# Kernel optimization log

Measured on AMD Instinct MI355X. Metric: run time of the kernel, lower is better.

The kernel has to match this reference:

```python
import jax, jax.numpy as jnp
import numpy as np

B, C, H, W = 4, 512, 64, 64
D = 512  # model_dim


def setup_inputs() -> dict:
    key = jax.random.key(0)
    ks = jax.random.split(key, 9)
    s = 0.02
    return {
        "q": jax.random.normal(ks[0], (B, C, H, W), dtype=jnp.float32),
        "Wq": jax.random.normal(ks[1], (D, C), dtype=jnp.float32) * s,
        "bq": jax.random.normal(ks[2], (D,), dtype=jnp.float32) * s,
        "Wk": jax.random.normal(ks[3], (D, C), dtype=jnp.float32) * s,
        "bk": jax.random.normal(ks[4], (D,), dtype=jnp.float32) * s,
        "Wv": jax.random.normal(ks[5], (D, C), dtype=jnp.float32) * s,
        "bv": jax.random.normal(ks[6], (D,), dtype=jnp.float32) * s,
        "Wo": jax.random.normal(ks[7], (C, D), dtype=jnp.float32) * s,
        "bo": jax.random.normal(ks[8], (C,), dtype=jnp.float32) * s,
    }


def reference(q, Wq, bq, Wk, bk, Wv, bv, Wo, bo):
    b, c, h, w = q.shape
    # 1x1 conv == per-pixel linear over channels; tokens s = h*w
    x = q.reshape(b, c, h * w)                      # (b, c, s)
    Q = jnp.einsum('bcs,dc->bsd', x, Wq) + bq       # (b, s, D)
    K = jnp.einsum('bcs,dc->bsd', x, Wk) + bk
    V = jnp.einsum('bcs,dc->bsd', x, Wv) + bv
    # ScaleAttend: scale = q.shape[-1]^-0.5 = model_dim^-0.5 (heads not split)
    scale = jnp.asarray(Q.shape[-1], Q.dtype) ** -0.5
    sim = jnp.einsum('bsd,btd->bst', Q, K) * scale  # (b, s, s)
    attn = jax.nn.softmax(sim, axis=-1)
    o = jnp.einsum('bst,btd->bsd', attn, V)         # (b, s, D)
    # to_out 1x1 conv: D -> C
    y = jnp.einsum('bsd,cd->bsc', o, Wo) + bo       # (b, s, C)
    return y.transpose(0, 2, 1).reshape(b, c, h, w)
```

## Files before the change

### kernel.cpp

```cpp
#include <hip/hip_runtime.h>
#include <hip/hip_bf16.h>

typedef __hip_bfloat16 bf16;
typedef __attribute__((ext_vector_type(8))) short short8;
typedef __attribute__((ext_vector_type(4))) float floatx4;
typedef __attribute__((ext_vector_type(4))) short shortx4;

static constexpr int BATCH = 4;
static constexpr int CH    = 512;
static constexpr int SEQ   = 4096;
static constexpr int DM    = 512;

__device__ __forceinline__ void gload16(const void* g, void* l) {
  __builtin_amdgcn_global_load_lds(
      (const __attribute__((address_space(1))) unsigned int*)g,
      (__attribute__((address_space(3))) unsigned int*)l,
      16, 0, 0);
}

__device__ __forceinline__ float hw_exp2(float x) {
  float r;
  asm("v_exp_f32 %0, %1" : "=v"(r) : "v"(x));
  return r;
}

__global__ __launch_bounds__(256) void cvt_weights(
    const float* __restrict__ w0, const float* __restrict__ w1,
    const float* __restrict__ w2, const float* __restrict__ w3,
    bf16* __restrict__ out) {
  const float* src = (blockIdx.y == 0) ? w0 : (blockIdx.y == 1) ? w1
                   : (blockIdx.y == 2) ? w2 : w3;
  int idx = blockIdx.x * 256 + threadIdx.x;
  out[(long)blockIdx.y * (DM * CH) + idx] = __float2bfloat16(src[idx]);
}

__global__ __launch_bounds__(256) void transpose_cvt(
    const float* __restrict__ x, bf16* __restrict__ xT) {
  __shared__ float tile[64][65];
  const int s0 = blockIdx.x * 64, c0 = blockIdx.y * 64;
  const float* xb = x + (long)blockIdx.z * CH * SEQ;
  bf16* xTb = xT + (long)blockIdx.z * SEQ * CH;
  const int t = threadIdx.x;
  const int sl = t & 63, cq = t >> 6;
  #pragma unroll
  for (int i = 0; i < 16; ++i) {
    int cl = cq * 16 + i;
    tile[cl][sl] = xb[(long)(c0 + cl) * SEQ + s0 + sl];
  }
  __syncthreads();
  const int cl2 = t & 63, sq = t >> 6;
  #pragma unroll
  for (int i = 0; i < 16; ++i) {
    int sl2 = sq * 16 + i;
    xTb[(long)(s0 + sl2) * CH + c0 + cl2] = __float2bfloat16(tile[cl2][sl2]);
  }
}

__global__ __launch_bounds__(512, 2) void gemm_qk(
    const bf16* __restrict__ A, long sAz,
    const bf16* __restrict__ B, long sBz,
    bf16* __restrict__ C, long sCz,
    float scale, int K, int ldc) {
  __shared__ __align__(16) bf16 As[2][256 * 64];
  __shared__ __align__(16) bf16 Bs[2][256 * 64];

  int id = blockIdx.x + gridDim.x * (blockIdx.y + gridDim.y * blockIdx.z);
  int nwg = gridDim.x * gridDim.y * gridDim.z;
  int sid = ((nwg & 7) == 0) ? ((id & 7) * (nwg >> 3) + (id >> 3)) : id;
  const int bx = sid % gridDim.x;
  const int by = (sid / gridDim.x) % gridDim.y;
  const int bz = sid / (gridDim.x * gridDim.y);

  const int tid = threadIdx.x;
  const long lK = K;
  const bf16* Ab = A + (long)bz * sAz + (long)by * 256 * lK;
  const bf16* Bb = B + (long)bz * sBz + (long)bx * 256 * lK;

  const int w = tid >> 6, lane = tid & 63;
  const int wr = w >> 2, wc = w & 3;
  const int l16 = lane & 15, quad = lane >> 4;

  const int srow = tid >> 3;
  const int sp = tid & 7;
  const int slog = (sp ^ (srow & 7)) << 3;

  const int pA0 = (quad ^ (l16 & 7)) << 3;
  const int pA1 = pA0 ^ 32;

  auto stage_half = [&](const bf16* Gb, bf16* Lb, int kt, int h) {
    #pragma unroll
    for (int r = 0; r < 2; ++r) {
      const int row = h * 128 + r * 64 + srow;
      gload16(Gb + (long)kt * 64 + (long)row * lK + slog,
              (char*)Lb + row * 128 + sp * 16);
    }
  };

  floatx4 acc[8][4];
  #pragma unroll
  for (int m = 0; m < 8; ++m)
    #pragma unroll
    for (int n = 0; n < 4; ++n) acc[m][n] = (floatx4)(0.0f);

  const int nk = K >> 6;
  stage_half(Ab, &As[0][0], 0, 0); stage_half(Bb, &Bs[0][0], 0, 0);
  stage_half(Ab, &As[0][0], 0, 1); stage_half(Bb, &Bs[0][0], 0, 1);
  if (nk > 1) { stage_half(Ab, &As[1][0], 1, 0); stage_half(Bb, &Bs[1][0], 1, 0); }
  asm volatile("s_waitcnt vmcnt(4)" ::: "memory");
  __builtin_amdgcn_s_barrier();

  for (int tt = 0; tt < nk; tt += 2) {
    #pragma unroll
    for (int u = 0; u < 2; ++u) {
      const bf16* __restrict__ Al = &As[u][0];
      const bf16* __restrict__ Bl = &Bs[u][0];
      short8 a[2][4], b[2][2][2];
      #pragma unroll
      for (int p = 0; p < 4; ++p) {
        const int rm = p >> 1, cn = p & 1;
        if (cn == 0) {
          #pragma unroll
          for (int kc = 0; kc < 2; ++kc)
            #pragma unroll
            for (int i = 0; i < 4; ++i)
              a[kc][i] = *(const short8*)(
                  Al + (rm * 128 + wr * 64 + i * 16 + l16) * 64
                     + (kc ? pA1 : pA0));
        }
        if (rm == 0) {
          #pragma unroll
          for (int kc = 0; kc < 2; ++kc)
            #pragma unroll
            for (int j = 0; j < 2; ++j)
              b[kc][cn][j] = *(const short8*)(
                  Bl + (cn * 128 + wc * 32 + j * 16 + l16) * 64
                     + (kc ? pA1 : pA0));
        }
        {
          const int g = u * 4 + p;
          const int stile = tt + 1 + ((g + 2) >> 2);
          if (stile < nk) {
            const int sh = (p < 2) ? 1 : 0;
            if (p & 1) stage_half(Bb, &Bs[stile & 1][0], stile, sh);
            else       stage_half(Ab, &As[stile & 1][0], stile, sh);
          }
        }
        __builtin_amdgcn_sched_barrier(0);
        __builtin_amdgcn_s_barrier();
        asm volatile("s_waitcnt lgkmcnt(0)" ::: "memory");
        __builtin_amdgcn_sched_barrier(0);
        __builtin_amdgcn_s_setprio(1);
        #pragma unroll
        for (int kc = 0; kc < 2; ++kc)
          #pragma unroll
          for (int i = 0; i < 4; ++i)
            #pragma unroll
            for (int j = 0; j < 2; ++j)
              acc[rm * 4 + i][cn * 2 + j] =
                  __builtin_amdgcn_mfma_f32_16x16x32_bf16(
                      a[kc][i], b[kc][cn][j], acc[rm * 4 + i][cn * 2 + j],
                      0, 0, 0);
        __builtin_amdgcn_s_setprio(0);
        if (p == 3) {
          if (u == 0) {
            if (tt + 2 < nk) asm volatile("s_waitcnt vmcnt(4)" ::: "memory");
            else             asm volatile("s_waitcnt vmcnt(0)" ::: "memory");
          } else {
            if (tt + 2 < nk) asm volatile("s_waitcnt vmcnt(4)" ::: "memory");
          }
        }
        __builtin_amdgcn_s_barrier();
      }
    }
  }

  bf16* Cb = C + (long)bz * sCz;
  #pragma unroll
  for (int rm = 0; rm < 2; ++rm)
    #pragma unroll
    for (int i = 0; i < 4; ++i) {
      const int row = by * 256 + rm * 128 + wr * 64 + i * 16 + quad * 4;
      #pragma unroll
      for (int cn = 0; cn < 2; ++cn)
        #pragma unroll
        for (int j = 0; j < 2; ++j) {
          const int col = bx * 256 + cn * 128 + wc * 32 + j * 16 + l16;
          floatx4 v = acc[rm * 4 + i][cn * 2 + j];
          #pragma unroll
          for (int r = 0; r < 4; ++r)
            Cb[(long)(row + r) * ldc + col] = __float2bfloat16(v[r] * scale);
        }
    }
}

__global__ __launch_bounds__(512, 2) void fused_smpv(
    const bf16* __restrict__ Sim, const bf16* __restrict__ Vt,
    bf16* __restrict__ Ob) {
  __shared__ __align__(16) bf16 Apv[2][64 * 64];
  __shared__ __align__(16) bf16 Bpv[2][512 * 64];
  __shared__ float rl_lds[64];

  const int id = blockIdx.x + (blockIdx.y << 6);
  const int bz = (id >> 1) & 3;
  const int by = ((id >> 3) << 1) | (id & 1);

  const int tid = threadIdx.x;
  const bf16* Simb = Sim + (long)bz * ((long)SEQ * SEQ) + (long)(by * 64) * SEQ;
  const bf16* Vb   = Vt  + (long)bz * ((long)SEQ * CH);
  bf16* Obb        = Ob  + (long)bz * ((long)SEQ * CH) + (long)(by * 64) * CH;

  const int srow = tid >> 3;
  const int sp = tid & 7;
  const int slog = (sp ^ (srow & 7)) << 3;
  const int aswz = (sp ^ (srow & 7)) << 4;

  const int w = tid >> 6, lane = tid & 63;
  const int l16 = lane & 15, quad = lane >> 4;
  const int pA0 = (quad ^ (l16 & 7)) << 3;
  const int pA1 = pA0 ^ 32;

  float lsum = 0.f;

  auto stageB8 = [&](int buf, int kt) {
    const bf16* s = Vb + (long)srow * SEQ + kt * 64 + slog;
    char* d = (char*)(&Bpv[buf][0]) + tid * 16;
    #pragma unroll
    for (int r = 0; r < 8; ++r)
      gload16(s + (long)(r * 64) * SEQ, d + r * 8192);
  };
  auto writeA = [&](int buf, uint4 u) {
    const ushort* h = (const ushort*)&u;
    union { uint4 u4; ushort hh[8]; } pk;
    #pragma unroll
    for (int k2 = 0; k2 < 8; ++k2) {
      float f = __uint_as_float(((unsigned)h[k2]) << 16);
      float e = hw_exp2(f);
      lsum += e;
      __hip_bfloat16 pb = __float2bfloat16(e);
      pk.hh[k2] = *(const ushort*)&pb;
    }
    *(uint4*)((char*)(&Apv[buf][0]) + srow * 128 + aswz) = pk.u4;
  };

  {
    uint4 ua = *(const uint4*)(Simb + (long)srow * SEQ + sp * 8);
    stageB8(0, 0);
    writeA(0, ua);
  }
  __syncthreads();

  floatx4 acc[4][4];
  #pragma unroll
  for (int i = 0; i < 4; ++i)
    #pragma unroll
    for (int j = 0; j < 4; ++j) acc[i][j] = (floatx4)(0.0f);

  const int nk = SEQ >> 6;
  for (int t = 0; t < nk; ++t) {
    const int cur = t & 1, nxt = cur ^ 1;
    const bool more = (t + 1 < nk);
    uint4 un;
    if (more) {
      un = *(const uint4*)(Simb + (long)srow * SEQ + (t + 1) * 64 + sp * 8);
      stageB8(nxt, t + 1);
    }
    short8 a[2][4], b[2][4];
    #pragma unroll
    for (int kc = 0; kc < 2; ++kc) {
      const int poff = kc ? pA1 : pA0;
      #pragma unroll
      for (int i = 0; i < 4; ++i)
        a[kc][i] = *(const short8*)(&Apv[cur][0] + (i * 16 + l16) * 64 + poff);
      #pragma unroll
      for (int j = 0; j < 4; ++j)
        b[kc][j] = *(const short8*)(&Bpv[cur][0]
                                    + (w * 64 + j * 16 + l16) * 64 + poff);
    }
    __builtin_amdgcn_s_setprio(1);
    #pragma unroll
    for (int kc = 0; kc < 2; ++kc)
      #pragma unroll
      for (int i = 0; i < 4; ++i)
        #pragma unroll
        for (int j = 0; j < 4; ++j)
          acc[i][j] = __builtin_amdgcn_mfma_f32_16x16x32_bf16(
              a[kc][i], b[kc][j], acc[i][j], 0, 0, 0);
    __builtin_amdgcn_s_setprio(0);
    if (more) writeA(nxt, un);
    __syncthreads();
  }

  #pragma unroll
  for (int o = 1; o < 8; o <<= 1) lsum += __shfl_xor(lsum, o);
  if (sp == 0) rl_lds[srow] = 1.0f / lsum;
  __syncthreads();

  #pragma unroll
  for (int i = 0; i < 4; ++i) {
    #pragma unroll
    for (int j = 0; j < 4; ++j) {
      floatx4 v = acc[i][j];
      const int col = w * 64 + j * 16 + l16;
      #pragma unroll
      for (int r = 0; r < 4; ++r) {
        const int row = i * 16 + quad * 4 + r;
        Obb[(long)row * CH + col] = __float2bfloat16(v[r] * rl_lds[row]);
      }
    }
  }
}

template <int MODE>
__global__ __launch_bounds__(512, 2) void gemm_bn128(
    const bf16* __restrict__ A, long sAz,
    const bf16* __restrict__ B, long sBz,
    void* __restrict__ Cv, long sCz,
    const float* __restrict__ bias, float scale,
    int K, int ldc) {
  __shared__ __align__(16) bf16 As[3][256 * 64];
  __shared__ __align__(16) bf16 Bs[3][128 * 64];

  int id = blockIdx.x + gridDim.x * (blockIdx.y + gridDim.y * blockIdx.z);
  int nwg = gridDim.x * gridDim.y * gridDim.z;
  int sid = ((nwg & 7) == 0) ? ((id & 7) * (nwg >> 3) + (id >> 3)) : id;
  const int bx = sid % gridDim.x;
  const int by = (sid / gridDim.x) % gridDim.y;
  const int bz = sid / (gridDim.x * gridDim.y);

  const int tid = threadIdx.x;
  const long lK = K;
  const bf16* Ab = A + (long)bz * sAz + (long)by * 256 * lK;
  const bf16* Bb = B + (long)bz * sBz + (long)bx * 128 * lK;

  const int w = tid >> 6, lane = tid & 63;
  const int wr = w >> 1, wc = w & 1;
  const int l16 = lane & 15, quad = lane >> 4;

  const int srow = tid >> 3;
  const int sp = tid & 7;
  const int slog = (sp ^ (srow & 7)) << 3;

  const int pA0 = (quad ^ (l16 & 7)) << 3;
  const int pA1 = pA0 ^ 32;

  auto stageA = [&](int buf, int kt) {
    const bf16* s = Ab + (long)kt * 64 + (long)srow * lK + slog;
    char* d = (char*)(&As[buf][0]) + tid * 16;
    #pragma unroll
    for (int r = 0; r < 4; ++r)
      gload16(s + (long)(r * 64) * lK, d + r * 8192);
  };
  auto stageB = [&](int buf, int kt) {
    const bf16* s = Bb + (long)kt * 64 + (long)srow * lK + slog;
    char* d = (char*)(&Bs[buf][0]) + tid * 16;
    #pragma unroll
    for (int r = 0; r < 2; ++r)
      gload16(s + (long)(r * 64) * lK, d + r * 8192);
  };

  floatx4 acc[4][4];
  #pragma unroll
  for (int m = 0; m < 4; ++m)
    #pragma unroll
    for (int n = 0; n < 4; ++n) acc[m][n] = (floatx4)(0.0f);

  const int nk = K >> 6;
  stageA(0, 0); stageB(0, 0);
  stageA(1, 1); stageB(1, 1);
  asm volatile("s_waitcnt vmcnt(6)" ::: "memory");
  __builtin_amdgcn_s_barrier();

  int bcur = 0, bstage = 2;
  for (int t = 0; t < nk; ++t) {
    const bf16* __restrict__ Al = &As[bcur][0];
    const bf16* __restrict__ Bl = &Bs[bcur][0];
    const bool more = (t + 2 < nk);
    #pragma unroll
    for (int kc = 0; kc < 2; ++kc) {
      const int poff = kc ? pA1 : pA0;
      short8 a[4], b[4];
      #pragma unroll
      for (int i = 0; i < 4; ++i)
        a[i] = *(const short8*)(Al + (wr * 64 + i * 16 + l16) * 64 + poff);
      #pragma unroll
      for (int j = 0; j < 4; ++j)
        b[j] = *(const short8*)(Bl + (wc * 64 + j * 16 + l16) * 64 + poff);
      if (more) {
        if (kc == 0) stageA(bstage, t + 2);
        else         stageB(bstage, t + 2);
      }
      __builtin_amdgcn_s_barrier();
      __builtin_amdgcn_s_setprio(1);
      #pragma unroll
      for (int i = 0; i < 4; ++i)
        #pragma unroll
        for (int j = 0; j < 4; ++j)
          acc[i][j] = __builtin_amdgcn_mfma_f32_16x16x32_bf16(
              a[i], b[j], acc[i][j], 0, 0, 0);
      __builtin_amdgcn_s_setprio(0);
      if (kc == 1) {
        if (more)            asm volatile("s_waitcnt vmcnt(6)" ::: "memory");
        else if (t + 1 < nk) asm volatile("s_waitcnt vmcnt(0)" ::: "memory");
      }
      __builtin_amdgcn_s_barrier();
    }
    bcur = (bcur == 2) ? 0 : bcur + 1;
    bstage = (bstage == 2) ? 0 : bstage + 1;
  }

  const int rbase = by * 256 + wr * 64 + quad * 4;
  const int cbase = bx * 128 + wc * 64 + l16;
  #pragma unroll
  for (int m = 0; m < 4; ++m) {
    const int row = rbase + m * 16;
    #pragma unroll
    for (int n = 0; n < 4; ++n) {
      const int col = cbase + n * 16;
      floatx4 v = acc[m][n];
      if constexpr (MODE == 0) {
        bf16* C = (bf16*)Cv + (long)bz * sCz;
        const float bb = bias[col];
        #pragma unroll
        for (int r = 0; r < 4; ++r)
          C[(long)(row + r) * ldc + col] = __float2bfloat16(v[r] + bb);
      } else if constexpr (MODE == 1) {
        bf16* C = (bf16*)Cv + (long)bz * sCz;
        const float bb = bias[col];
        alignas(8) bf16 tmp[4];
        #pragma unroll
        for (int r = 0; r < 4; ++r) tmp[r] = __float2bfloat16(v[r] + bb);
        *(shortx4*)(C + (long)col * ldc + row) = *(const shortx4*)tmp;
      } else {
        float* C = (float*)Cv + (long)bz * sCz;
        const float bb = bias[col];
        floatx4 o_;
        #pragma unroll
        for (int r = 0; r < 4; ++r) o_[r] = v[r] + bb;
        *(floatx4*)(C + (long)col * ldc + row) = o_;
      }
    }
  }
}

extern "C" void kernel_launch(void* const* d_in, const int* in_sizes, int n_in,
                              void* d_out, int out_size, void* d_ws,
                              size_t ws_size, hipStream_t stream) {
  const float* q  = (const float*)d_in[0];
  const float* Wq = (const float*)d_in[1];
  const float* bq = (const float*)d_in[2];
  const float* Wk = (const float*)d_in[3];
  const float* bk = (const float*)d_in[4];
  const float* Wv = (const float*)d_in[5];
  const float* bv = (const float*)d_in[6];
  const float* Wo = (const float*)d_in[7];
  const float* bo = (const float*)d_in[8];
  float* out = (float*)d_out;

  bf16* ws = (bf16*)d_ws;
  const long WSZ = (long)DM * CH;
  const long XSZ = (long)SEQ * CH;
  const long SSZ = (long)SEQ * SEQ;
  bf16* Wqb = ws;
  bf16* Wkb = Wqb + WSZ;
  bf16* Wvb = Wqb + 2 * WSZ;
  bf16* Wob = Wqb + 3 * WSZ;
  bf16* xT  = Wqb + 4 * WSZ;
  bf16* Qb  = xT + BATCH * XSZ;
  bf16* Kb  = Qb + BATCH * XSZ;
  bf16* Vt  = Kb + BATCH * XSZ;
  bf16* Ob  = Vt + BATCH * XSZ;
  bf16* Sim = Ob + BATCH * XSZ;

  cvt_weights<<<dim3(WSZ / 256, 4), 256, 0, stream>>>(Wq, Wk, Wv, Wo, ws);
  transpose_cvt<<<dim3(SEQ / 64, CH / 64, BATCH), 256, 0, stream>>>(q, xT);

  gemm_bn128<0><<<dim3(4, 16, BATCH), 512, 0, stream>>>(
      xT, XSZ, Wqb, 0, Qb, XSZ, bq, 1.f, CH, DM);
  gemm_bn128<0><<<dim3(4, 16, BATCH), 512, 0, stream>>>(
      xT, XSZ, Wkb, 0, Kb, XSZ, bk, 1.f, CH, DM);
  gemm_bn128<1><<<dim3(4, 16, BATCH), 512, 0, stream>>>(
      xT, XSZ, Wvb, 0, Vt, XSZ, bv, 1.f, CH, SEQ);
  const float qkscale = 0.04419417382415922f * 1.4426950408889634f;
  gemm_qk<<<dim3(16, 16, BATCH), 512, 0, stream>>>(
      Qb, XSZ, Kb, XSZ, Sim, SSZ, qkscale, CH, SEQ);
  fused_smpv<<<dim3(64, 4), 512, 0, stream>>>(Sim, Vt, Ob);
  gemm_bn128<4><<<dim3(4, 16, BATCH), 512, 0, stream>>>(
      Ob, XSZ, Wob, 0, out, XSZ, bo, 1.f, DM, SEQ);
}
```

Baseline: 352.6 us.

## Fuse Q/K/V projections into one launch with smaller 128x128 tiles

Replaces the three separate Q, K and V projection GEMM launches with one proj128 launch whose z dimension selects the weight matrix, bias and output layout (V written transposed). Tiles shrink from 256x128 with 512 threads and triple buffering to 128x128 with 256 threads and double buffering, giving more workgroups per launch to fill the CUs. The output projection uses the same kernel. The fused_smpv batch index expression is also rewritten, though it computes the same value. The shallower pipeline and the extra syncthreads per k-step may expose more load latency.

```diff
diff --git a/kernel.cpp b/kernel.cpp
--- a/kernel.cpp
+++ b/kernel.cpp
@@ -53,6 +53,127 @@
   for (int i = 0; i < 16; ++i) {
     int sl2 = sq * 16 + i;
     xTb[(long)(s0 + sl2) * CH + c0 + cl2] = __float2bfloat16(tile[cl2][sl2]);
+  }
+}
+
+template <int KIND>
+__global__ __launch_bounds__(256, 2) void proj128(
+    const bf16* __restrict__ A0, const bf16* __restrict__ Wbase,
+    const float* __restrict__ b0, const float* __restrict__ b1,
+    const float* __restrict__ b2, void* __restrict__ Cbase) {
+  __shared__ __align__(16) bf16 As[2][128 * 64];
+  __shared__ __align__(16) bf16 Bs[2][128 * 64];
+
+  int id = blockIdx.x + gridDim.x * (blockIdx.y + gridDim.y * blockIdx.z);
+  int nwg = gridDim.x * gridDim.y * gridDim.z;
+  int sid = ((nwg & 7) == 0) ? ((id & 7) * (nwg >> 3) + (id >> 3)) : id;
+  const int bx = sid % gridDim.x;
+  const int by = (sid / gridDim.x) % gridDim.y;
+  const int z  = sid / (gridDim.x * gridDim.y);
+  const int mat = (KIND == 0) ? (z >> 2) : 0;
+  const int bz  = (KIND == 0) ? (z & 3) : z;
+
+  const long XSZ = (long)SEQ * CH;
+  const long lK = CH;
+  const bf16* Ab = A0 + (long)bz * XSZ + (long)by * 128 * lK;
+  const bf16* Bb = Wbase + (long)mat * ((long)DM * CH) + (long)bx * 128 * lK;
+  const float* bias = (KIND == 1) ? b0 : (mat == 0 ? b0 : mat == 1 ? b1 : b2);
+
+  const int tid = threadIdx.x;
+  const int w = tid >> 6, lane = tid & 63;
+  const int wr = w >> 1, wc = w & 1;
+  const int l16 = lane & 15, quad = lane >> 4;
+  const int srow = tid >> 3;
+  const int sp = tid & 7;
+  const int slog = (sp ^ (srow & 7)) << 3;
+  const int pA0 = (quad ^ (l16 & 7)) << 3;
+  const int pA1 = pA0 ^ 32;
+
+  auto stageA = [&](int buf, int kt) {
+    const bf16* s = Ab + kt * 64 + (long)srow * lK + slog;
+    char* d = (char*)(&As[buf][0]) + tid * 16;
+    #pragma unroll
+    for (int r = 0; r < 4; ++r)
+      gload16(s + (long)(r * 32) * lK, d + r * 4096);
+  };
+  auto stageB = [&](int buf, int kt) {
+    const bf16* s = Bb + kt * 64 + (long)srow * lK + slog;
+    char* d = (char*)(&Bs[buf][0]) + tid * 16;
+    #pragma unroll
+    for (int r = 0; r < 4; ++r)
+      gload16(s + (long)(r * 32) * lK, d + r * 4096);
+  };
+
+  floatx4 acc[4][4];
+  #pragma unroll
+  for (int m = 0; m < 4; ++m)
+    #pragma unroll
+    for (int n = 0; n < 4; ++n) acc[m][n] = (floatx4)(0.0f);
+
+  const int nk = CH >> 6;
+  stageA(0, 0); stageB(0, 0);
+  __syncthreads();
+
+  for (int t = 0; t < nk; ++t) {
+    const int cur = t & 1, nxt = cur ^ 1;
+    const bool more = (t + 1 < nk);
+    #pragma unroll
+    for (int kc = 0; kc < 2; ++kc) {
+      const int poff = kc ? pA1 : pA0;
+      short8 a[4], b[4];
+      #pragma unroll
+      for (int i = 0; i < 4; ++i)
+        a[i] = *(const short8*)(&As[cur][0] + (wr * 64 + i * 16 + l16) * 64 + poff);
+      #pragma unroll
+      for (int j = 0; j < 4; ++j)
+        b[j] = *(const short8*)(&Bs[cur][0] + (wc * 64 + j * 16 + l16) * 64 + poff);
+      if (more) {
+        if (kc == 0) stageA(nxt, t + 1);
+        else         stageB(nxt, t + 1);
+      }
+      __builtin_amdgcn_s_setprio(1);
+      #pragma unroll
+      for (int i = 0; i < 4; ++i)
+        #pragma unroll
+        for (int j = 0; j < 4; ++j)
+          acc[i][j] = __builtin_amdgcn_mfma_f32_16x16x32_bf16(
+              a[i], b[j], acc[i][j], 0, 0, 0);
+      __builtin_amdgcn_s_setprio(0);
+    }
+    __syncthreads();
+  }
+
+  const int rbase = by * 128 + wr * 64 + quad * 4;
+  const int cbase = bx * 128 + wc * 64 + l16;
+  #pragma unroll
+  for (int m = 0; m < 4; ++m) {
+    const int row = rbase + m * 16;
+    #pragma unroll
+    for (int n = 0; n < 4; ++n) {
+      const int col = cbase + n * 16;
+      floatx4 v = acc[m][n];
+      const float bb = bias[col];
+      if constexpr (KIND == 0) {
+        if (mat < 2) {
+          bf16* C = (bf16*)Cbase + (long)mat * (BATCH * XSZ) + (long)bz * XSZ;
+          #pragma unroll
+          for (int r = 0; r < 4; ++r)
+            C[(long)(row + r) * DM + col] = __float2bfloat16(v[r] + bb);
+        } else {
+          bf16* C = (bf16*)Cbase + 2 * (BATCH * XSZ) + (long)bz * XSZ;
+          alignas(8) bf16 tmp[4];
+          #pragma unroll
+          for (int r = 0; r < 4; ++r) tmp[r] = __float2bfloat16(v[r] + bb);
+          *(shortx4*)(C + (long)col * SEQ + row) = *(const shortx4*)tmp;
+        }
+      } else {
+        float* C = (float*)Cbase + (long)bz * XSZ;
+        floatx4 o_;
+        #pragma unroll
+        for (int r = 0; r < 4; ++r) o_[r] = v[r] + bb;
+        *(floatx4*)(C + (long)col * SEQ + row) = o_;
+      }
+    }
   }
 }
 
@@ -201,7 +322,8 @@
   __shared__ float rl_lds[64];
 
   const int id = blockIdx.x + (blockIdx.y << 6);
-  const int bz = (id >> 1) & 3;
+  const int xcd = id & 7;
+  const int bz = xcd >> 1;
   const int by = ((id >> 3) << 1) | (id & 1);
 
   const int tid = threadIdx.x;
@@ -305,138 +427,6 @@
       for (int r = 0; r < 4; ++r) {
         const int row = i * 16 + quad * 4 + r;
         Obb[(long)row * CH + col] = __float2bfloat16(v[r] * rl_lds[row]);
-      }
-    }
-  }
-}
-
-template <int MODE>
-__global__ __launch_bounds__(512, 2) void gemm_bn128(
-    const bf16* __restrict__ A, long sAz,
-    const bf16* __restrict__ B, long sBz,
-    void* __restrict__ Cv, long sCz,
-    const float* __restrict__ bias, float scale,
-    int K, int ldc) {
-  __shared__ __align__(16) bf16 As[3][256 * 64];
-  __shared__ __align__(16) bf16 Bs[3][128 * 64];
-
-  int id = blockIdx.x + gridDim.x * (blockIdx.y + gridDim.y * blockIdx.z);
-  int nwg = gridDim.x * gridDim.y * gridDim.z;
-  int sid = ((nwg & 7) == 0) ? ((id & 7) * (nwg >> 3) + (id >> 3)) : id;
-  const int bx = sid % gridDim.x;
-  const int by = (sid / gridDim.x) % gridDim.y;
-  const int bz = sid / (gridDim.x * gridDim.y);
-
-  const int tid = threadIdx.x;
-  const long lK = K;
-  const bf16* Ab = A + (long)bz * sAz + (long)by * 256 * lK;
-  const bf16* Bb = B + (long)bz * sBz + (long)bx * 128 * lK;
-
-  const int w = tid >> 6, lane = tid & 63;
-  const int wr = w >> 1, wc = w & 1;
-  const int l16 = lane & 15, quad = lane >> 4;
-
-  const int srow = tid >> 3;
-  const int sp = tid & 7;
-  const int slog = (sp ^ (srow & 7)) << 3;
-
-  const int pA0 = (quad ^ (l16 & 7)) << 3;
-  const int pA1 = pA0 ^ 32;
-
-  auto stageA = [&](int buf, int kt) {
-    const bf16* s = Ab + (long)kt * 64 + (long)srow * lK + slog;
-    char* d = (char*)(&As[buf][0]) + tid * 16;
-    #pragma unroll
-    for (int r = 0; r < 4; ++r)
-      gload16(s + (long)(r * 64) * lK, d + r * 8192);
-  };
-  auto stageB = [&](int buf, int kt) {
-    const bf16* s = Bb + (long)kt * 64 + (long)srow * lK + slog;
-    char* d = (char*)(&Bs[buf][0]) + tid * 16;
-    #pragma unroll
-    for (int r = 0; r < 2; ++r)
-      gload16(s + (long)(r * 64) * lK, d + r * 8192);
-  };
-
-  floatx4 acc[4][4];
-  #pragma unroll
-  for (int m = 0; m < 4; ++m)
-    #pragma unroll
-    for (int n = 0; n < 4; ++n) acc[m][n] = (floatx4)(0.0f);
-
-  const int nk = K >> 6;
-  stageA(0, 0); stageB(0, 0);
-  stageA(1, 1); stageB(1, 1);
-  asm volatile("s_waitcnt vmcnt(6)" ::: "memory");
-  __builtin_amdgcn_s_barrier();
-
-  int bcur = 0, bstage = 2;
-  for (int t = 0; t < nk; ++t) {
-    const bf16* __restrict__ Al = &As[bcur][0];
-    const bf16* __restrict__ Bl = &Bs[bcur][0];
-    const bool more = (t + 2 < nk);
-    #pragma unroll
-    for (int kc = 0; kc < 2; ++kc) {
-      const int poff = kc ? pA1 : pA0;
-      short8 a[4], b[4];
-      #pragma unroll
-      for (int i = 0; i < 4; ++i)
-        a[i] = *(const short8*)(Al + (wr * 64 + i * 16 + l16) * 64 + poff);
-      #pragma unroll
-      for (int j = 0; j < 4; ++j)
-        b[j] = *(const short8*)(Bl + (wc * 64 + j * 16 + l16) * 64 + poff);
-      if (more) {
-        if (kc == 0) stageA(bstage, t + 2);
-        else         stageB(bstage, t + 2);
-      }
-      __builtin_amdgcn_s_barrier();
-      __builtin_amdgcn_s_setprio(1);
-      #pragma unroll
-      for (int i = 0; i < 4; ++i)
-        #pragma unroll
-        for (int j = 0; j < 4; ++j)
-          acc[i][j] = __builtin_amdgcn_mfma_f32_16x16x32_bf16(
-              a[i], b[j], acc[i][j], 0, 0, 0);
-      __builtin_amdgcn_s_setprio(0);
-      if (kc == 1) {
-        if (more)            asm volatile("s_waitcnt vmcnt(6)" ::: "memory");
-        else if (t + 1 < nk) asm volatile("s_waitcnt vmcnt(0)" ::: "memory");
-      }
-      __builtin_amdgcn_s_barrier();
-    }
-    bcur = (bcur == 2) ? 0 : bcur + 1;
-    bstage = (bstage == 2) ? 0 : bstage + 1;
-  }
-
-  const int rbase = by * 256 + wr * 64 + quad * 4;
-  const int cbase = bx * 128 + wc * 64 + l16;
-  #pragma unroll
-  for (int m = 0; m < 4; ++m) {
-    const int row = rbase + m * 16;
-    #pragma unroll
-    for (int n = 0; n < 4; ++n) {
-      const int col = cbase + n * 16;
-      floatx4 v = acc[m][n];
-      if constexpr (MODE == 0) {
-        bf16* C = (bf16*)Cv + (long)bz * sCz;
-        const float bb = bias[col];
-        #pragma unroll
-        for (int r = 0; r < 4; ++r)
-          C[(long)(row + r) * ldc + col] = __float2bfloat16(v[r] + bb);
-      } else if constexpr (MODE == 1) {
-        bf16* C = (bf16*)Cv + (long)bz * sCz;
-        const float bb = bias[col];
-        alignas(8) bf16 tmp[4];
-        #pragma unroll
-        for (int r = 0; r < 4; ++r) tmp[r] = __float2bfloat16(v[r] + bb);
-        *(shortx4*)(C + (long)col * ldc + row) = *(const shortx4*)tmp;
-      } else {
-        float* C = (float*)Cv + (long)bz * sCz;
-        const float bb = bias[col];
-        floatx4 o_;
-        #pragma unroll
-        for (int r = 0; r < 4; ++r) o_[r] = v[r] + bb;
-        *(floatx4*)(C + (long)col * ldc + row) = o_;
       }
     }
   }
@@ -461,8 +451,6 @@
   const long XSZ = (long)SEQ * CH;
   const long SSZ = (long)SEQ * SEQ;
   bf16* Wqb = ws;
-  bf16* Wkb = Wqb + WSZ;
-  bf16* Wvb = Wqb + 2 * WSZ;
   bf16* Wob = Wqb + 3 * WSZ;
   bf16* xT  = Wqb + 4 * WSZ;
   bf16* Qb  = xT + BATCH * XSZ;
@@ -474,16 +462,12 @@
   cvt_weights<<<dim3(WSZ / 256, 4), 256, 0, stream>>>(Wq, Wk, Wv, Wo, ws);
   transpose_cvt<<<dim3(SEQ / 64, CH / 64, BATCH), 256, 0, stream>>>(q, xT);
 
-  gemm_bn128<0><<<dim3(4, 16, BATCH), 512, 0, stream>>>(
-      xT, XSZ, Wqb, 0, Qb, XSZ, bq, 1.f, CH, DM);
-  gemm_bn128<0><<<dim3(4, 16, BATCH), 512, 0, stream>>>(
-      xT, XSZ, Wkb, 0, Kb, XSZ, bk, 1.f, CH, DM);
-  gemm_bn128<1><<<dim3(4, 16, BATCH), 512, 0, stream>>>(
-      xT, XSZ, Wvb, 0, Vt, XSZ, bv, 1.f, CH, SEQ);
+  proj128<0><<<dim3(4, 32, 12), 256, 0, stream>>>(
+      xT, Wqb, bq, bk, bv, Qb);
   const float qkscale = 0.04419417382415922f * 1.4426950408889634f;
   gemm_qk<<<dim3(16, 16, BATCH), 512, 0, stream>>>(
       Qb, XSZ, Kb, XSZ, Sim, SSZ, qkscale, CH, SEQ);
   fused_smpv<<<dim3(64, 4), 512, 0, stream>>>(Sim, Vt, Ob);
-  gemm_bn128<4><<<dim3(4, 16, BATCH), 512, 0, stream>>>(
-      Ob, XSZ, Wob, 0, out, XSZ, bo, 1.f, DM, SEQ);
-}
+  proj128<1><<<dim3(4, 32, 4), 256, 0, stream>>>(
+      Ob, Wob, bo, nullptr, nullptr, out);
+}
```

New measurement: 342.6 us (median of 2 runs). 1.03x faster.
